# Optimization experiments

Hardware: AMD Instinct MI355X
Metric: run time of the kernel (lower is better)

The kernel has to match this reference:

```python
import jax, jax.numpy as jnp
import numpy as np

H, HKV, D, HID = 32, 8, 128, 4096
EPS = 1e-6
ROPE_BASE = 10000.0
SCALE = D ** -0.5


def setup_inputs() -> dict:
    key = jax.random.key(0)
    ks = jax.random.split(key, 4)
    T = 2048
    x = jax.random.normal(ks[0], (T, HID), dtype=jnp.float32)
    w_qkv = jax.random.normal(ks[1], ((H + 2 * HKV) * D, HID), dtype=jnp.float32) * (HID ** -0.5)
    b_qkv = jax.random.normal(ks[2], ((H + 2 * HKV) * D,), dtype=jnp.float32) * 0.02
    q_norm_w = jnp.ones((D,), dtype=jnp.float32)
    k_norm_w = jnp.ones((D,), dtype=jnp.float32)
    w_o = jax.random.normal(ks[3], (HID, H * D), dtype=jnp.float32) * ((H * D) ** -0.5)
    return {"x": x, "w_qkv": w_qkv, "b_qkv": b_qkv, "q_norm_w": q_norm_w,
            "k_norm_w": k_norm_w, "w_o": w_o}


def _rms_norm(t, w):
    # per-head RMSNorm over the last (head_dim) axis
    var = jnp.mean(t * t, axis=-1, keepdims=True)
    return t * jax.lax.rsqrt(var + EPS) * w


def _rope(t, cos, sin):
    # neox-style half rotation; cos/sin: [T, D//2], t: [T, h, D]
    t1, t2 = jnp.split(t, 2, axis=-1)
    c = cos[:, None, :]
    s = sin[:, None, :]
    return jnp.concatenate([t1 * c - t2 * s, t2 * c + t1 * s], axis=-1)


def reference(x, w_qkv, b_qkv, q_norm_w, k_norm_w, w_o):
    T = x.shape[0]
    qkv = x @ w_qkv.T + b_qkv                      # [T, (H+2*HKV)*D]
    q, k, v = jnp.split(qkv, [H * D, (H + HKV) * D], axis=-1)
    q = q.reshape(T, H, D)
    k = k.reshape(T, HKV, D)
    v = v.reshape(T, HKV, D)

    # QK RMSNorm
    q = _rms_norm(q, q_norm_w)
    k = _rms_norm(k, k_norm_w)

    # rotary embedding, base 10000, full head_dim
    pos = jnp.arange(T, dtype=jnp.float32)
    inv_freq = 1.0 / (ROPE_BASE ** (jnp.arange(0, D, 2, dtype=jnp.float32) / D))
    freqs = pos[:, None] * inv_freq[None, :]        # [T, D//2]
    cos, sin = jnp.cos(freqs), jnp.sin(freqs)
    q = _rope(q, cos, sin)
    k = _rope(k, cos, sin)

    # GQA: kv_head_mapping = arange(HKV).repeat_interleave(H // HKV)
    groups = H // HKV
    k = jnp.repeat(k, groups, axis=1)               # [T, H, D]
    v = jnp.repeat(v, groups, axis=1)

    scores = jnp.einsum('thd,shd->hts', q, k) * SCALE   # [H, T, T]
    causal = jnp.tril(jnp.ones((T, T), dtype=bool))
    scores = jnp.where(causal[None], scores, jnp.finfo(scores.dtype).min)
    probs = jax.nn.softmax(scores, axis=-1)
    out = jnp.einsum('hts,shd->thd', probs, v)      # [T, H, D]
    return out.reshape(T, H * D) @ w_o.T            # [T, HID]
```

## Files before the change

kernel.cpp:

```cpp
#include <hip/hip_runtime.h>
#include <stdint.h>
#include <stddef.h>

typedef __bf16 bf16_t;
typedef __bf16 bf16x8 __attribute__((ext_vector_type(8)));
typedef float  f32x4  __attribute__((ext_vector_type(4)));

#define T_SEQ 2048
#define NH    32
#define NKV   8
#define DH    128
#define HIDN  4096
#define NQKV  6144
#define SCALE 0.08838834764831845f
#define MBOUND 11.5f

__device__ inline float b2f(bf16_t v) {
  uint32_t u = ((uint32_t)__builtin_bit_cast(uint16_t, v)) << 16;
  return __builtin_bit_cast(float, u);
}
__device__ inline bf16_t f2b(float f) { return (bf16_t)f; }
__device__ inline void gl_lds16(const void* g, void* l) {
  __builtin_amdgcn_global_load_lds(
      (__attribute__((address_space(1))) void*)g,
      (__attribute__((address_space(3))) void*)l, 16, 0, 0);
}
__device__ inline f32x4 mfma16(bf16x8 a, bf16x8 b, f32x4 c) {
  return __builtin_amdgcn_mfma_f32_16x16x32_bf16(a, b, c, 0, 0, 0);
}
__device__ inline void store_val(float* p, float v)  { *p = v; }
__device__ inline void store_val(bf16_t* p, float v) { *p = f2b(v); }

__global__ __launch_bounds__(256)
void cvt_kernel(const float* __restrict__ in, bf16_t* __restrict__ out) {
  size_t i = ((size_t)blockIdx.x * 256 + threadIdx.x) * 8;
  f32x4 a = *(const f32x4*)(in + i);
  f32x4 b = *(const f32x4*)(in + i + 4);
  bf16x8 o;
#pragma unroll
  for (int e = 0; e < 4; ++e) { o[e] = f2b(a[e]); o[e + 4] = f2b(b[e]); }
  *(bf16x8*)(out + i) = o;
}

template <bool BIAS, typename TOUT>
__global__ __launch_bounds__(256)
void gemm_bt(const bf16_t* __restrict__ A, const bf16_t* __restrict__ Bw,
             const float* __restrict__ bias, TOUT* __restrict__ C,
             int M, int N, int K) {
  __shared__ __align__(16) char smem[32768];
  char* sA = smem;
  char* sB = smem + 16384;
  const int tid  = threadIdx.x;
  const int lane = tid & 63, wave = tid >> 6;
  const int quad = lane >> 4, l16 = lane & 15;
  const int wm = wave >> 1, wn = wave & 1;
  const int m0 = blockIdx.y * 128, n0 = blockIdx.x * 128;

  f32x4 acc[4][4] = {};
  const int kTiles = K >> 6;

  for (int kt = 0; kt < kTiles; ++kt) {
    const int kb = kt << 6;
#pragma unroll
    for (int i = 0; i < 4; ++i) {
      int p = i * 256 + tid;
      int row = p >> 3, gc = (p & 7) ^ (row & 7);
      gl_lds16(A  + (size_t)(m0 + row) * K + kb + gc * 8, sA + p * 16);
      gl_lds16(Bw + (size_t)(n0 + row) * K + kb + gc * 8, sB + p * 16);
    }
    __syncthreads();

#pragma unroll
    for (int ks = 0; ks < 2; ++ks) {
      bf16x8 af[4], bfr[4];
      const int c = ks * 4 + quad;
#pragma unroll
      for (int i = 0; i < 4; ++i) {
        int ra = wm * 64 + i * 16 + l16;
        af[i]  = *(const bf16x8*)(sA + ra * 128 + ((c ^ (ra & 7)) * 16));
        int rb = wn * 64 + i * 16 + l16;
        bfr[i] = *(const bf16x8*)(sB + rb * 128 + ((c ^ (rb & 7)) * 16));
      }
#pragma unroll
      for (int i = 0; i < 4; ++i)
#pragma unroll
        for (int j = 0; j < 4; ++j)
          acc[i][j] = mfma16(af[i], bfr[j], acc[i][j]);
    }
    __syncthreads();
  }
#pragma unroll
  for (int i = 0; i < 4; ++i) {
    int mrow = m0 + wm * 64 + i * 16 + quad * 4;
#pragma unroll
    for (int j = 0; j < 4; ++j) {
      int ncol = n0 + wn * 64 + j * 16 + l16;
      float bv = BIAS ? bias[ncol] : 0.f;
#pragma unroll
      for (int r = 0; r < 4; ++r)
        store_val(&C[(size_t)(mrow + r) * N + ncol], acc[i][j][r] + bv);
    }
  }
}

__global__ __launch_bounds__(256)
void prep_kernel(const bf16_t* __restrict__ qkv, const float* __restrict__ qw,
                 const float* __restrict__ kw, bf16_t* __restrict__ Qp,
                 bf16_t* __restrict__ Kp, bf16_t* __restrict__ Vp) {
  const int id   = blockIdx.x * 4 + (threadIdx.x >> 6);
  const int lane = threadIdx.x & 63;
  const int t = id / 48, slot = id % 48;
  const bf16_t* src = qkv + (size_t)t * NQKV + slot * DH;
  float x1 = b2f(src[lane]), x2 = b2f(src[lane + 64]);
  float o1, o2;
  if (slot < 40) {
    float ssq = x1 * x1 + x2 * x2;
#pragma unroll
    for (int m = 1; m < 64; m <<= 1) ssq += __shfl_xor(ssq, m, 64);
    float rms = rsqrtf(ssq * (1.f / 128.f) + 1e-6f);
    const float* w = (slot < 32) ? qw : kw;
    float n1 = x1 * rms * w[lane];
    float n2 = x2 * rms * w[lane + 64];
    float inv = exp2f(-0.20762050593046014f * (float)lane);
    float ang = (float)t * inv;
    float cs = cosf(ang), sn = sinf(ang);
    o1 = n1 * cs - n2 * sn;
    o2 = n2 * cs + n1 * sn;
  } else { o1 = x1; o2 = x2; }
  bf16_t* dst;
  if (slot < 32)      dst = Qp + ((size_t)t * NH  + slot)        * DH;
  else if (slot < 40) dst = Kp + ((size_t)t * NKV + (slot - 32)) * DH;
  else                dst = Vp + ((size_t)t * NKV + (slot - 40)) * DH;
  dst[lane] = f2b(o1); dst[lane + 64] = f2b(o2);
}

__global__ __launch_bounds__(256)
void vtrans_kernel(const bf16_t* __restrict__ Vp, bf16_t* __restrict__ Vt) {
  __shared__ bf16_t tile[64 * 66];
  const int t0 = blockIdx.x * 64, d0 = blockIdx.y * 64, kvh = blockIdx.z;
  const int tid = threadIdx.x;
#pragma unroll
  for (int i = 0; i < 2; ++i) {
    int id = i * 256 + tid;
    int tr = id >> 3, dc = id & 7;
    bf16x8 v = *(const bf16x8*)(Vp + ((size_t)(t0 + tr) * NKV + kvh) * DH + d0 + dc * 8);
#pragma unroll
    for (int e = 0; e < 8; ++e) tile[tr * 66 + dc * 8 + e] = v[e];
  }
  __syncthreads();
#pragma unroll
  for (int i = 0; i < 2; ++i) {
    int id = i * 256 + tid;
    int dr = id >> 3, tc = id & 7;
    bf16x8 o;
#pragma unroll
    for (int e = 0; e < 8; ++e) o[e] = tile[(tc * 8 + e) * 66 + dr];
    *(bf16x8*)(Vt + ((size_t)kvh * DH + d0 + dr) * T_SEQ + t0 + tc * 8) = o;
  }
}

__global__ __launch_bounds__(256)
void attn_kernel(const bf16_t* __restrict__ Qp, const bf16_t* __restrict__ Kp,
                 const bf16_t* __restrict__ Vt, bf16_t* __restrict__ Out) {
  __shared__ __align__(16) char smem[73728];
  const int tid  = threadIdx.x;
  const int lane = tid & 63, wave = tid >> 6;
  const int quad = lane >> 4, l16 = lane & 15;
  const int b = blockIdx.x, h = blockIdx.y;
  const int qt_lo = b, qt_hi = 31 - b;
  const int kvh = h >> 2;
  char* sPw = smem + 65536 + wave * 2048;

  bf16x8 qf_lo[4], qf_hi[4];
  {
    const int row_lo = qt_lo * 64 + wave * 16 + l16;
    const int row_hi = qt_hi * 64 + wave * 16 + l16;
#pragma unroll
    for (int ks = 0; ks < 4; ++ks) {
      qf_lo[ks] = *(const bf16x8*)(Qp + ((size_t)row_lo * NH + h) * DH + ks * 32 + quad * 8);
      qf_hi[ks] = *(const bf16x8*)(Qp + ((size_t)row_hi * NH + h) * DH + ks * 32 + quad * 8);
    }
  }
  f32x4 acc_lo[8] = {}, acc_hi[8] = {};
  float l_lo[4] = {0.f, 0.f, 0.f, 0.f}, l_hi[4] = {0.f, 0.f, 0.f, 0.f};

  auto stage = [&](int kt) {
    char* sK = smem + (kt & 1) * 16384;
    char* sV = smem + 32768 + (kt & 1) * 16384;
    const int k0 = kt * 64;
#pragma unroll
    for (int i = 0; i < 4; ++i) {
      int p = i * 256 + tid;
      int row = p >> 4, gc = (p & 15) ^ (row & 15);
      gl_lds16(Kp + ((size_t)(k0 + row) * NKV + kvh) * DH + gc * 8, sK + p * 16);
    }
#pragma unroll
    for (int i = 0; i < 4; ++i) {
      int p = i * 256 + tid;
      int d = p >> 3, gc = (p & 7) ^ (d & 7);
      gl_lds16(Vt + ((size_t)kvh * DH + d) * T_SEQ + k0 + gc * 8, sV + p * 16);
    }
  };

  auto compute = [&](const bf16x8 (&qf)[4], f32x4 (&acc)[8], float (&lrow)[4],
                     int qt, int kt, char* sK, char* sVT) {
    f32x4 sfr[4] = {};
#pragma unroll
    for (int ks = 0; ks < 4; ++ks) {
      const int c = ks * 4 + quad;
#pragma unroll
      for (int j = 0; j < 4; ++j) {
        int row = j * 16 + l16;
        bf16x8 kf = *(const bf16x8*)(sK + row * 256 + ((c ^ (row & 15)) * 16));
        sfr[j] = mfma16(qf[ks], kf, sfr[j]);
      }
    }
    float sv[4][4];
    const bool diag = (kt == qt);
#pragma unroll
    for (int j = 0; j < 4; ++j)
#pragma unroll
      for (int r = 0; r < 4; ++r) {
        float e = __expf(fmaf(sfr[j][r], SCALE, -MBOUND));
        if (diag) {
          int qg = wave * 16 + quad * 4 + r;
          int kg = j * 16 + l16;
          if (kg > qg) e = 0.f;
        }
        sv[j][r] = e;
      }
#pragma unroll
    for (int r = 0; r < 4; ++r)
      lrow[r] += (sv[0][r] + sv[1][r]) + (sv[2][r] + sv[3][r]);
#pragma unroll
    for (int j = 0; j < 4; ++j)
#pragma unroll
      for (int r = 0; r < 4; ++r) {
        int prow = quad * 4 + r;
        int col  = j * 16 + l16;
        int c    = col >> 3;
        ((bf16_t*)(sPw + prow * 128 + ((c ^ (prow & 7)) * 16)))[col & 7] = f2b(sv[j][r]);
      }
    __asm__ volatile("" ::: "memory");
    bf16x8 pf[2];
#pragma unroll
    for (int ks2 = 0; ks2 < 2; ++ks2) {
      int c = ks2 * 4 + quad;
      pf[ks2] = *(const bf16x8*)(sPw + l16 * 128 + ((c ^ (l16 & 7)) * 16));
    }
    __asm__ volatile("" ::: "memory");
#pragma unroll
    for (int j2 = 0; j2 < 8; ++j2)
#pragma unroll
      for (int ks2 = 0; ks2 < 2; ++ks2) {
        int d = j2 * 16 + l16;
        int c = ks2 * 4 + quad;
        bf16x8 vf = *(const bf16x8*)(sVT + d * 128 + ((c ^ (d & 7)) * 16));
        acc[j2] = mfma16(pf[ks2], vf, acc[j2]);
      }
  };

  stage(0);
  for (int kt = 0; kt <= qt_hi; ++kt) {
    __syncthreads();
    if (kt < qt_hi) stage(kt + 1);
    char* sK  = smem + (kt & 1) * 16384;
    char* sVT = smem + 32768 + (kt & 1) * 16384;
    compute(qf_hi, acc_hi, l_hi, qt_hi, kt, sK, sVT);
    if (kt <= qt_lo)
      compute(qf_lo, acc_lo, l_lo, qt_lo, kt, sK, sVT);
  }

#pragma unroll
  for (int r = 0; r < 4; ++r) {
    float lh = l_hi[r], ll = l_lo[r];
#pragma unroll
    for (int m = 1; m < 16; m <<= 1) {
      lh += __shfl_xor(lh, m, 64);
      ll += __shfl_xor(ll, m, 64);
    }
    float inv_h = 1.f / lh, inv_l = 1.f / ll;
    int qg_h = qt_hi * 64 + wave * 16 + quad * 4 + r;
    int qg_l = qt_lo * 64 + wave * 16 + quad * 4 + r;
#pragma unroll
    for (int j2 = 0; j2 < 8; ++j2) {
      int d = j2 * 16 + l16;
      Out[(size_t)qg_h * (NH * DH) + h * DH + d] = f2b(acc_hi[j2][r] * inv_h);
      Out[(size_t)qg_l * (NH * DH) + h * DH + d] = f2b(acc_lo[j2][r] * inv_l);
    }
  }
}

extern "C" void kernel_launch(void* const* d_in, const int* in_sizes, int n_in,
                              void* d_out, int out_size, void* d_ws, size_t ws_size,
                              hipStream_t stream) {
  const float* x    = (const float*)d_in[0];
  const float* wqkv = (const float*)d_in[1];
  const float* bqkv = (const float*)d_in[2];
  const float* qnw  = (const float*)d_in[3];
  const float* knw  = (const float*)d_in[4];
  const float* wo   = (const float*)d_in[5];
  float* out = (float*)d_out;

  char* ws = (char*)d_ws;
  bf16_t* wqkvb = (bf16_t*)(ws);
  bf16_t* xb    = (bf16_t*)(ws + 50331648);
  bf16_t* qkv   = (bf16_t*)(ws + 67108864);
  bf16_t* Qp    = (bf16_t*)(ws);
  bf16_t* Kp    = (bf16_t*)(ws + 16777216);
  bf16_t* Vp    = (bf16_t*)(ws + 20971520);
  bf16_t* Vt    = (bf16_t*)(ws + 25165824);
  bf16_t* wob   = (bf16_t*)(ws + 29360128);
  bf16_t* At    = (bf16_t*)(ws + 67108864);

  cvt_kernel<<<(T_SEQ * HIDN) / 2048, 256, 0, stream>>>(x, xb);
  cvt_kernel<<<(NQKV * HIDN) / 2048, 256, 0, stream>>>(wqkv, wqkvb);
  gemm_bt<true, bf16_t><<<dim3(NQKV / 128, T_SEQ / 128), 256, 0, stream>>>(
      xb, wqkvb, bqkv, qkv, T_SEQ, NQKV, HIDN);
  prep_kernel<<<(T_SEQ * 48) / 4, 256, 0, stream>>>(qkv, qnw, knw, Qp, Kp, Vp);
  vtrans_kernel<<<dim3(T_SEQ / 64, DH / 64, NKV), 256, 0, stream>>>(Vp, Vt);
  cvt_kernel<<<(HIDN * HIDN) / 2048, 256, 0, stream>>>(wo, wob);
  attn_kernel<<<dim3(16, NH), 256, 0, stream>>>(Qp, Kp, Vt, At);
  gemm_bt<false, float><<<dim3(HIDN / 128, T_SEQ / 128), 256, 0, stream>>>(
      At, wob, nullptr, out, T_SEQ, HIDN, HIDN);
}
```

Measured before the change: 515.9 us.

## Merge input conversions, use fast trig/exp2, and prioritize MFMA waves in attention

Merges the x and w_qkv fp32-to-bf16 conversions into a single launch. Replaces cosf/sinf with the fast intrinsics in the rope prep and rewrites the softmax exponential as exp2 with the scale and log2(e) constants folded in. Adds s_setprio around the QK and PV MFMA loops in the attention kernel so waves issuing matrix ops get scheduling priority. Fast trig loses some accuracy at large angles, which could matter for positions up to 2047.

```diff
diff --git a/kernel.cpp b/kernel.cpp
--- a/kernel.cpp
+++ b/kernel.cpp
@@ -14,6 +14,8 @@
 #define NQKV  6144
 #define SCALE 0.08838834764831845f
 #define MBOUND 11.5f
+#define C1_EXP2 0.12751743187767f
+#define C2_EXP2 16.590992970223f
 
 __device__ inline float b2f(bf16_t v) {
   uint32_t u = ((uint32_t)__builtin_bit_cast(uint16_t, v)) << 16;
@@ -30,6 +32,24 @@
 }
 __device__ inline void store_val(float* p, float v)  { *p = v; }
 __device__ inline void store_val(bf16_t* p, float v) { *p = f2b(v); }
+
+__global__ __launch_bounds__(256)
+void cvt2_kernel(const float* __restrict__ a, bf16_t* __restrict__ ao, int na,
+                 const float* __restrict__ b, bf16_t* __restrict__ bo) {
+  int blk = blockIdx.x;
+  const float* in;
+  bf16_t* out;
+  int rb;
+  if (blk < na) { in = a; out = ao; rb = blk; }
+  else          { in = b; out = bo; rb = blk - na; }
+  size_t i = ((size_t)rb * 256 + threadIdx.x) * 8;
+  f32x4 va = *(const f32x4*)(in + i);
+  f32x4 vb = *(const f32x4*)(in + i + 4);
+  bf16x8 o;
+#pragma unroll
+  for (int e = 0; e < 4; ++e) { o[e] = f2b(va[e]); o[e + 4] = f2b(vb[e]); }
+  *(bf16x8*)(out + i) = o;
+}
 
 __global__ __launch_bounds__(256)
 void cvt_kernel(const float* __restrict__ in, bf16_t* __restrict__ out) {
@@ -123,7 +143,7 @@
     float n2 = x2 * rms * w[lane + 64];
     float inv = exp2f(-0.20762050593046014f * (float)lane);
     float ang = (float)t * inv;
-    float cs = cosf(ang), sn = sinf(ang);
+    float cs = __cosf(ang), sn = __sinf(ang);
     o1 = n1 * cs - n2 * sn;
     o2 = n2 * cs + n1 * sn;
   } else { o1 = x1; o2 = x2; }
@@ -205,6 +225,7 @@
   auto compute = [&](const bf16x8 (&qf)[4], f32x4 (&acc)[8], float (&lrow)[4],
                      int qt, int kt, char* sK, char* sVT) {
     f32x4 sfr[4] = {};
+    __builtin_amdgcn_s_setprio(1);
 #pragma unroll
     for (int ks = 0; ks < 4; ++ks) {
       const int c = ks * 4 + quad;
@@ -215,13 +236,14 @@
         sfr[j] = mfma16(qf[ks], kf, sfr[j]);
       }
     }
+    __builtin_amdgcn_s_setprio(0);
     float sv[4][4];
     const bool diag = (kt == qt);
 #pragma unroll
     for (int j = 0; j < 4; ++j)
 #pragma unroll
       for (int r = 0; r < 4; ++r) {
-        float e = __expf(fmaf(sfr[j][r], SCALE, -MBOUND));
+        float e = exp2f(fmaf(sfr[j][r], C1_EXP2, -C2_EXP2));
         if (diag) {
           int qg = wave * 16 + quad * 4 + r;
           int kg = j * 16 + l16;
@@ -249,6 +271,7 @@
       pf[ks2] = *(const bf16x8*)(sPw + l16 * 128 + ((c ^ (l16 & 7)) * 16));
     }
     __asm__ volatile("" ::: "memory");
+    __builtin_amdgcn_s_setprio(1);
 #pragma unroll
     for (int j2 = 0; j2 < 8; ++j2)
 #pragma unroll
@@ -258,6 +281,7 @@
         bf16x8 vf = *(const bf16x8*)(sVT + d * 128 + ((c ^ (d & 7)) * 16));
         acc[j2] = mfma16(pf[ks2], vf, acc[j2]);
       }
+    __builtin_amdgcn_s_setprio(0);
   };
 
   stage(0);
@@ -313,8 +337,7 @@
   bf16_t* wob   = (bf16_t*)(ws + 29360128);
   bf16_t* At    = (bf16_t*)(ws + 67108864);
 
-  cvt_kernel<<<(T_SEQ * HIDN) / 2048, 256, 0, stream>>>(x, xb);
-  cvt_kernel<<<(NQKV * HIDN) / 2048, 256, 0, stream>>>(wqkv, wqkvb);
+  cvt2_kernel<<<16384, 256, 0, stream>>>(x, xb, 4096, wqkv, wqkvb);
   gemm_bt<true, bf16_t><<<dim3(NQKV / 128, T_SEQ / 128), 256, 0, stream>>>(
       xb, wqkvb, bqkv, qkv, T_SEQ, NQKV, HIDN);
   prep_kernel<<<(T_SEQ * 48) / 4, 256, 0, stream>>>(qkv, qnw, knw, Qp, Kp, Vp);
```

Measured after the change: 533.6 us. 1.03x slower.
